# Kernel tuning notes

Measured on AMD Instinct MI355X. Metric: run time of the kernel, lower is better.

## Reference

```python
import jax, jax.numpy as jnp
import numpy as np

SEQ = 4096
R_DIM = 1024
Z_DIM = 1024
AT_DIM = 1024
G_DIM = 1024


def _xavier(key, shape):
    fan_in, fan_out = shape[1], shape[0]
    limit = float(np.sqrt(6.0 / (fan_in + fan_out)))
    return jax.random.uniform(key, shape, jnp.float32, -limit, limit)


def setup_inputs() -> dict:
    key = jax.random.key(0)
    ks = jax.random.split(key, 12)
    return {
        "R": jax.random.normal(ks[0], (SEQ, R_DIM), jnp.float32),
        "W_alpha": _xavier(ks[1], (R_DIM, 2 * R_DIM)),
        "b_alpha": jnp.zeros((R_DIM,), jnp.float32),
        "W_delta": _xavier(ks[2], (R_DIM, 2 * R_DIM)),
        "b_delta": jnp.zeros((R_DIM,), jnp.float32),
        "W_q": _xavier(ks[3], (AT_DIM, Z_DIM)),
        "b_q": jnp.zeros((AT_DIM,), jnp.float32),
        "W_k": _xavier(ks[4], (AT_DIM, Z_DIM)),
        "b_k": jnp.zeros((AT_DIM,), jnp.float32),
        "W_v": _xavier(ks[5], (AT_DIM, Z_DIM)),
        "b_v": jnp.zeros((AT_DIM,), jnp.float32),
        "W_z": _xavier(ks[6], (Z_DIM, R_DIM)),
        "b_z": jnp.zeros((Z_DIM,), jnp.float32),
        "W_f": _xavier(ks[7], (AT_DIM, G_DIM)),
        "b_f": jnp.zeros((AT_DIM,), jnp.float32),
        "W_EMA": _xavier(ks[8], (G_DIM, R_DIM)),
        "b_EMA": jnp.zeros((G_DIM,), jnp.float32),
        "W_z_at": _xavier(ks[9], (G_DIM, AT_DIM)),
        "b_z_at": jnp.zeros((G_DIM,), jnp.float32),
        "W_i": _xavier(ks[10], (1, R_DIM)),
        "b_i": jnp.zeros((1,), jnp.float32),
        "W_final": _xavier(ks[11], (1, G_DIM)),
    }


def reference(R, W_alpha, b_alpha, W_delta, b_delta, W_q, b_q, W_k, b_k,
              W_v, b_v, W_z, b_z, W_f, b_f, W_EMA, b_EMA, W_z_at, b_z_at,
              W_i, b_i, W_final):
    r_dim = R.shape[-1]
    at_dim = W_q.shape[0]
    # prepend zero row; r_t / r_{t-1} pairs
    R2 = jnp.concatenate([jnp.zeros((1, r_dim), R.dtype), R], axis=0)
    r_t, r_prev = R2[1:], R2[:-1]
    concat_r = jnp.concatenate([r_prev, r_t], axis=1)  # [m, 2r]
    alpha = jnp.tanh(concat_r @ W_alpha.T + b_alpha)
    delta = jnp.tanh(concat_r @ W_delta.T + b_delta)
    R_EMA = alpha * r_t + (1.0 - alpha) * delta * r_prev
    Z = jax.nn.silu(R_EMA @ W_z.T + b_z)
    Q = Z @ W_q.T + b_q
    K = Z @ W_k.T + b_k
    V = Z @ W_v.T + b_v
    scores = (Q @ K.T) / jnp.sqrt(jnp.float32(at_dim))  # [m, m]
    weights = jax.nn.softmax(scores, axis=-1)
    Z_at = weights @ V
    R_EMA_p = R_EMA @ W_EMA.T + b_EMA
    f = jax.nn.sigmoid(R_EMA_p @ W_f.T + b_f)
    Z_at_p = f * Z_at
    Z_EMA_f = Z_at_p @ W_z_at.T + b_z_at
    Z_tp = jnp.tanh(R_EMA_p + Z_EMA_f)
    i = jnp.tanh(R_EMA @ W_i.T + b_i)  # [m, 1]
    Z_final = i * Z_tp + (1.0 - i) * R_EMA_p
    p_hat = jax.nn.sigmoid(Z_final @ W_final.T)  # [m, 1]
    return p_hat
```

## Files before the change

kernel.cpp:

```cpp
#include <hip/hip_runtime.h>
#include <cstdint>
#include <cmath>

#define MB (1024ull * 1024ull)

typedef unsigned short u16;
typedef __attribute__((ext_vector_type(8))) short short8;
typedef __attribute__((ext_vector_type(4))) float f32x4;

enum { M_TANH = 0, M_ZRE = 1, M_QKV = 2, M_SIG = 3, M_SCALE = 4, M_PVMUL = 5, M_F32 = 6 };

__device__ __forceinline__ u16 f2b(float f) {
  union { float f; uint32_t u; } v; v.f = f;
  uint32_t r = v.u + 0x7FFFu + ((v.u >> 16) & 1u);
  return (u16)(r >> 16);
}
__device__ __forceinline__ float b2f(u16 u) {
  union { uint32_t u; float f; } v; v.u = ((uint32_t)u) << 16;
  return v.f;
}

typedef __attribute__((address_space(3))) uint32_t lds_u32;
typedef const __attribute__((address_space(1))) uint32_t glb_u32;

__device__ __forceinline__ void gload16(const void* g, void* l) {
  __builtin_amdgcn_global_load_lds((glb_u32*)g, (lds_u32*)l, 16, 0, 0);
}

template <int MODE, int BNT>
__global__ __launch_bounds__(256) void gemm(const u16* __restrict__ A,
                                            const u16* __restrict__ B,
                                            const float* __restrict__ bias,
                                            const u16* __restrict__ auxb,
                                            u16* __restrict__ Cb,
                                            u16* __restrict__ Cb2,
                                            float* __restrict__ Cf,
                                            int K, int lda, int ldb, float scale) {
  constexpr int NJ = (BNT == 128) ? 4 : 2;
  __shared__ u16 As[2][128 * 32];
  __shared__ u16 Bs[2][BNT * 32];
  const int tid = threadIdx.x;
  const int wid = tid >> 6, lane = tid & 63;

  const int gx = gridDim.x, nwg = gx * gridDim.y;
  int id = blockIdx.y * gx + blockIdx.x;
  if ((nwg & 7) == 0) id = (id & 7) * (nwg >> 3) + (id >> 3);
  const int bm = (id / gx) * 128, bn = (id % gx) * BNT;
  const int wm = wid >> 1, wn = wid & 1;

  const int srow = tid >> 2;
  const int schunk = (tid & 3) ^ ((srow >> 1) & 3);
  const u16* gA = A + (size_t)(bm + srow) * lda + schunk * 8;
  const u16* gB = B + (size_t)(bn + srow) * ldb + schunk * 8;

  f32x4 acc[4][NJ];
#pragma unroll
  for (int i = 0; i < 4; ++i)
#pragma unroll
    for (int j = 0; j < NJ; ++j) acc[i][j] = (f32x4){0.f, 0.f, 0.f, 0.f};

  const int ar = lane & 15;
  const int pch = (((lane >> 4) ^ ((ar >> 1) & 3))) * 8;

  const int NT = K >> 5;

  auto stage = [&](int buf, int t) {
    const u16* a = gA + (size_t)t * 32;
    const u16* b = gB + (size_t)t * 32;
    gload16(a, &As[buf][wid * 512]);
    gload16(a + (size_t)64 * lda, &As[buf][wid * 512 + 2048]);
    gload16(b, &Bs[buf][wid * 512]);
    if (BNT == 128) gload16(b + (size_t)64 * ldb, &Bs[buf][wid * 512 + 2048]);
  };

  stage(0, 0);
  __syncthreads();
  int cur = 0;
  for (int t = 0; t < NT; ++t) {
    if (t + 1 < NT) stage(cur ^ 1, t + 1);
    short8 af[4], bf[NJ];
#pragma unroll
    for (int i = 0; i < 4; ++i)
      af[i] = *reinterpret_cast<const short8*>(&As[cur][(wm * 64 + i * 16 + ar) * 32 + pch]);
#pragma unroll
    for (int j = 0; j < NJ; ++j)
      bf[j] = *reinterpret_cast<const short8*>(&Bs[cur][(wn * (BNT / 2) + j * 16 + ar) * 32 + pch]);
#pragma unroll
    for (int i = 0; i < 4; ++i)
#pragma unroll
      for (int j = 0; j < NJ; ++j)
        acc[i][j] = __builtin_amdgcn_mfma_f32_16x16x32_bf16(af[i], bf[j], acc[i][j], 0, 0, 0);
    __syncthreads();
    cur ^= 1;
  }

#pragma unroll
  for (int i = 0; i < 4; ++i) {
    const int rb = bm + wm * 64 + i * 16 + (lane >> 4) * 4;
#pragma unroll
    for (int j = 0; j < NJ; ++j) {
      const int n = bn + wn * (BNT / 2) + j * 16 + (lane & 15);
#pragma unroll
      for (int r = 0; r < 4; ++r) {
        const int m = rb + r;
        float v = acc[i][j][r];
        if (MODE == M_TANH) {
          v = tanhf(v + bias[n]);
          Cb[(size_t)m * 2048 + n] = f2b(v);
        } else if (MODE == M_ZRE) {
          v += bias[n];
          if (n < 1024) { const float s = v / (1.f + expf(-v)); Cb[(size_t)m * 1024 + n] = f2b(s); }
          else Cb2[(size_t)m * 1024 + (n - 1024)] = f2b(v);
        } else if (MODE == M_QKV) {
          v += bias[n];
          if (n < 2048) Cb[(size_t)m * 2048 + n] = f2b(v);
          else Cb2[(size_t)m * 1024 + (n - 2048)] = f2b(v);
        } else if (MODE == M_SIG) {
          v = 1.f / (1.f + expf(-(v + bias[n])));
          Cb[(size_t)m * 1024 + n] = f2b(v);
        } else if (MODE == M_SCALE) {
          Cb[(size_t)m * 4096 + n] = f2b(v * scale);
        } else if (MODE == M_PVMUL) {
          v *= b2f(auxb[(size_t)m * 1024 + n]);
          Cb[(size_t)m * 1024 + n] = f2b(v);
        } else if (MODE == M_F32) {
          Cf[(size_t)m * 1024 + n] = v + bias[n];
        }
      }
    }
  }
}

__global__ __launch_bounds__(256) void convert_all(
    const float* __restrict__ s0, const float* __restrict__ s1, const float* __restrict__ s2,
    const float* __restrict__ s3, const float* __restrict__ s4, const float* __restrict__ s5,
    const float* __restrict__ s6, const float* __restrict__ s7, const float* __restrict__ s8,
    u16* __restrict__ Wad, u16* __restrict__ Wze, u16* __restrict__ Wqkv,
    u16* __restrict__ Wfb, u16* __restrict__ Wzab) {
  const int idx = blockIdx.x * 256 + threadIdx.x;
  const float* src; u16* dst; int off;
  if      (idx < 524288)  { src = s0; dst = Wad;           off = idx; }
  else if (idx < 1048576) { src = s1; dst = Wad + 2097152; off = idx - 524288; }
  else if (idx < 1310720) { src = s2; dst = Wze;           off = idx - 1048576; }
  else if (idx < 1572864) { src = s3; dst = Wze + 1048576; off = idx - 1310720; }
  else if (idx < 1835008) { src = s4; dst = Wqkv;          off = idx - 1572864; }
  else if (idx < 2097152) { src = s5; dst = Wqkv + 1048576; off = idx - 1835008; }
  else if (idx < 2359296) { src = s6; dst = Wqkv + 2097152; off = idx - 2097152; }
  else if (idx < 2621440) { src = s7; dst = Wfb;           off = idx - 2359296; }
  else                    { src = s8; dst = Wzab;          off = idx - 2621440; }
  const float4 v = reinterpret_cast<const float4*>(src)[off];
  ushort4 o; o.x = f2b(v.x); o.y = f2b(v.y); o.z = f2b(v.z); o.w = f2b(v.w);
  reinterpret_cast<ushort4*>(dst)[off] = o;
}

__global__ void copy_bias(const float* __restrict__ ba, const float* __restrict__ bd,
                          const float* __restrict__ bz, const float* __restrict__ be,
                          const float* __restrict__ bq, const float* __restrict__ bk,
                          const float* __restrict__ bv,
                          float* __restrict__ bad, float* __restrict__ bze,
                          float* __restrict__ bqkv) {
  const int t = threadIdx.x;
  const float4* src; float4* dst;
  switch (blockIdx.x) {
    case 0: src = (const float4*)ba; dst = (float4*)bad; break;
    case 1: src = (const float4*)bd; dst = (float4*)(bad + 1024); break;
    case 2: src = (const float4*)bz; dst = (float4*)bze; break;
    case 3: src = (const float4*)be; dst = (float4*)(bze + 1024); break;
    case 4: src = (const float4*)bq; dst = (float4*)bqkv; break;
    case 5: src = (const float4*)bk; dst = (float4*)(bqkv + 1024); break;
    default: src = (const float4*)bv; dst = (float4*)(bqkv + 2048); break;
  }
  dst[t] = src[t];
}

__global__ __launch_bounds__(256) void concat_kern(const float* __restrict__ R,
                                                   u16* __restrict__ Rc) {
  const int idx = blockIdx.x * 256 + threadIdx.x;
  const int m = idx >> 9;
  const int c = (idx & 511) * 4;
  float4 v;
  if (c < 1024) {
    if (m > 0) v = *reinterpret_cast<const float4*>(&R[(size_t)(m - 1) * 1024 + c]);
    else v = make_float4(0.f, 0.f, 0.f, 0.f);
  } else {
    v = *reinterpret_cast<const float4*>(&R[(size_t)m * 1024 + (c - 1024)]);
  }
  ushort4 o; o.x = f2b(v.x); o.y = f2b(v.y); o.z = f2b(v.z); o.w = f2b(v.w);
  reinterpret_cast<ushort4*>(Rc)[idx] = o;
}

__global__ __launch_bounds__(256) void ema_combine(const float* __restrict__ R,
                                                   const u16* __restrict__ adb,
                                                   u16* __restrict__ REMA) {
  const int idx = blockIdx.x * 256 + threadIdx.x;
  const int m = idx >> 8, c4 = idx & 255;
  const float4 rt = reinterpret_cast<const float4*>(R)[idx];
  float4 rp = make_float4(0.f, 0.f, 0.f, 0.f);
  if (m > 0) rp = reinterpret_cast<const float4*>(R)[idx - 256];
  const ushort4 a4 = reinterpret_cast<const ushort4*>(adb)[m * 512 + c4];
  const ushort4 d4 = reinterpret_cast<const ushort4*>(adb)[m * 512 + 256 + c4];
  ushort4 o;
  { const float av = b2f(a4.x); o.x = f2b(av * rt.x + (1.f - av) * b2f(d4.x) * rp.x); }
  { const float av = b2f(a4.y); o.y = f2b(av * rt.y + (1.f - av) * b2f(d4.y) * rp.y); }
  { const float av = b2f(a4.z); o.z = f2b(av * rt.z + (1.f - av) * b2f(d4.z) * rp.z); }
  { const float av = b2f(a4.w); o.w = f2b(av * rt.w + (1.f - av) * b2f(d4.w) * rp.w); }
  reinterpret_cast<ushort4*>(REMA)[idx] = o;
}

__device__ __forceinline__ float waveMax(float v) {
#pragma unroll
  for (int o = 32; o; o >>= 1) v = fmaxf(v, __shfl_down(v, o));
  return v;
}
__device__ __forceinline__ float waveSum(float v) {
#pragma unroll
  for (int o = 32; o; o >>= 1) v += __shfl_down(v, o);
  return v;
}

__global__ __launch_bounds__(256) void softmax_rows(u16* __restrict__ S) {
  u16* p = S + (size_t)blockIdx.x * 4096;
  const int tid = threadIdx.x;
  float v[16];
#pragma unroll
  for (int j = 0; j < 4; ++j) {
    const ushort4 t = *reinterpret_cast<const ushort4*>(&p[tid * 4 + 1024 * j]);
    v[4 * j + 0] = b2f(t.x); v[4 * j + 1] = b2f(t.y);
    v[4 * j + 2] = b2f(t.z); v[4 * j + 3] = b2f(t.w);
  }
  float mx = -INFINITY;
#pragma unroll
  for (int j = 0; j < 16; ++j) mx = fmaxf(mx, v[j]);
  __shared__ float red[4];
  const float wm = waveMax(mx);
  if ((tid & 63) == 0) red[tid >> 6] = wm;
  __syncthreads();
  mx = fmaxf(fmaxf(red[0], red[1]), fmaxf(red[2], red[3]));
  __syncthreads();
  float sum = 0.f;
#pragma unroll
  for (int j = 0; j < 16; ++j) { v[j] = expf(v[j] - mx); sum += v[j]; }
  const float ws_ = waveSum(sum);
  if ((tid & 63) == 0) red[tid >> 6] = ws_;
  __syncthreads();
  const float inv = 1.f / (red[0] + red[1] + red[2] + red[3]);
#pragma unroll
  for (int j = 0; j < 4; ++j) {
    ushort4 t;
    t.x = f2b(v[4 * j + 0] * inv); t.y = f2b(v[4 * j + 1] * inv);
    t.z = f2b(v[4 * j + 2] * inv); t.w = f2b(v[4 * j + 3] * inv);
    *reinterpret_cast<ushort4*>(&p[tid * 4 + 1024 * j]) = t;
  }
}

__global__ __launch_bounds__(256) void transpose_b16(const u16* __restrict__ V,
                                                     u16* __restrict__ Vt) {
  __shared__ u16 t[64][72];
  const int bn = blockIdx.x * 64;
  const int bk = blockIdx.y * 64;
  const int tx = threadIdx.x & 15, ty = threadIdx.x >> 4;
#pragma unroll
  for (int i = 0; i < 64; i += 16) {
    const ushort4 v = *reinterpret_cast<const ushort4*>(&V[(size_t)(bk + ty + i) * 1024 + bn + tx * 4]);
    t[ty + i][tx * 4 + 0] = v.x; t[ty + i][tx * 4 + 1] = v.y;
    t[ty + i][tx * 4 + 2] = v.z; t[ty + i][tx * 4 + 3] = v.w;
  }
  __syncthreads();
#pragma unroll
  for (int i = 0; i < 64; i += 16) {
    ushort4 w;
    w.x = t[tx * 4 + 0][ty + i]; w.y = t[tx * 4 + 1][ty + i];
    w.z = t[tx * 4 + 2][ty + i]; w.w = t[tx * 4 + 3][ty + i];
    *reinterpret_cast<ushort4*>(&Vt[(size_t)(bn + ty + i) * 4096 + bk + tx * 4]) = w;
  }
}

__global__ void final_kern(const u16* __restrict__ REMAb, const u16* __restrict__ REMApb,
                           const float* __restrict__ ZEMAf,
                           const float* __restrict__ Wi, const float* __restrict__ bi,
                           const float* __restrict__ Wfin, float* __restrict__ out) {
  const int m = blockIdx.x, l = threadIdx.x;
  float si = 0.f;
#pragma unroll
  for (int j = 0; j < 16; ++j) {
    const int n = l + 64 * j;
    si += b2f(REMAb[(size_t)m * 1024 + n]) * Wi[n];
  }
#pragma unroll
  for (int o = 32; o; o >>= 1) si += __shfl_xor(si, o);
  const float im = tanhf(si + bi[0]);
  float s = 0.f;
#pragma unroll
  for (int j = 0; j < 16; ++j) {
    const int n = l + 64 * j;
    const float rp = b2f(REMApb[(size_t)m * 1024 + n]);
    const float zf = im * tanhf(rp + ZEMAf[(size_t)m * 1024 + n]) + (1.f - im) * rp;
    s += zf * Wfin[n];
  }
#pragma unroll
  for (int o = 32; o; o >>= 1) s += __shfl_down(s, o);
  if (l == 0) out[m] = 1.f / (1.f + expf(-s));
}

extern "C" void kernel_launch(void* const* d_in, const int* in_sizes, int n_in,
                              void* d_out, int out_size, void* d_ws, size_t ws_size,
                              hipStream_t stream) {
  const float* R       = (const float*)d_in[0];
  const float* W_alpha = (const float*)d_in[1];  const float* b_alpha = (const float*)d_in[2];
  const float* W_delta = (const float*)d_in[3];  const float* b_delta = (const float*)d_in[4];
  const float* W_q     = (const float*)d_in[5];  const float* b_q     = (const float*)d_in[6];
  const float* W_k     = (const float*)d_in[7];  const float* b_k     = (const float*)d_in[8];
  const float* W_v     = (const float*)d_in[9];  const float* b_v     = (const float*)d_in[10];
  const float* W_z     = (const float*)d_in[11]; const float* b_z     = (const float*)d_in[12];
  const float* W_f     = (const float*)d_in[13]; const float* b_f     = (const float*)d_in[14];
  const float* W_EMA   = (const float*)d_in[15]; const float* b_EMA   = (const float*)d_in[16];
  const float* W_z_at  = (const float*)d_in[17]; const float* b_z_at  = (const float*)d_in[18];
  const float* W_i     = (const float*)d_in[19]; const float* b_i     = (const float*)d_in[20];
  const float* W_final = (const float*)d_in[21];
  float* out = (float*)d_out;
  uint8_t* w8 = (uint8_t*)d_ws;

  u16*   Rc     = (u16*)(w8 + 0 * MB);
  u16*   Zb     = (u16*)(w8 + 0 * MB);
  u16*   REMApb = (u16*)(w8 + 8 * MB);
  u16*   Wad    = (u16*)(w8 + 16 * MB);
  u16*   fvb    = (u16*)(w8 + 16 * MB);
  u16*   adb    = (u16*)(w8 + 24 * MB);
  float* ZEMAf  = (float*)(w8 + 24 * MB);
  u16*   Wqkv   = (u16*)(w8 + 40 * MB);
  u16*   Vtb    = (u16*)(w8 + 40 * MB);
  u16*   Wze    = (u16*)(w8 + 46 * MB);
  u16*   Wfb    = (u16*)(w8 + 50 * MB);
  u16*   Wzab   = (u16*)(w8 + 52 * MB);
  u16*   REMAb  = (u16*)(w8 + 54 * MB);
  u16*   QKb    = (u16*)(w8 + 62 * MB);
  u16*   Zatpb  = (u16*)(w8 + 62 * MB);
  u16*   Vb     = (u16*)(w8 + 78 * MB);
  u16*   Sb     = (u16*)(w8 + 78 * MB);
  float* bad    = (float*)(w8 + 110 * MB + 64 * 1024);
  float* bze    = bad + 2048;
  float* bqkv   = bze + 2048;

  const dim3 blk(256);
  convert_all<<<11264, blk, 0, stream>>>(W_alpha, W_delta, W_z, W_EMA, W_q, W_k, W_v, W_f, W_z_at,
                                         Wad, Wze, Wqkv, Wfb, Wzab);
  concat_kern<<<8192, blk, 0, stream>>>(R, Rc);
  copy_bias<<<7, blk, 0, stream>>>(b_alpha, b_delta, b_z, b_EMA, b_q, b_k, b_v, bad, bze, bqkv);

  gemm<M_TANH, 128><<<dim3(16, 32), blk, 0, stream>>>(Rc, Wad, bad, nullptr, adb, nullptr, nullptr, 2048, 2048, 2048, 1.f);
  ema_combine<<<4096, blk, 0, stream>>>(R, adb, REMAb);
  gemm<M_ZRE, 128><<<dim3(16, 32), blk, 0, stream>>>(REMAb, Wze, bze, nullptr, Zb, REMApb, nullptr, 1024, 1024, 1024, 1.f);
  gemm<M_QKV, 128><<<dim3(24, 32), blk, 0, stream>>>(Zb, Wqkv, bqkv, nullptr, QKb, Vb, nullptr, 1024, 1024, 1024, 1.f);
  gemm<M_SIG, 64><<<dim3(16, 32), blk, 0, stream>>>(REMApb, Wfb, b_f, nullptr, fvb, nullptr, nullptr, 1024, 1024, 1024, 1.f);
  transpose_b16<<<dim3(16, 64), blk, 0, stream>>>(Vb, Vtb);
  gemm<M_SCALE, 128><<<dim3(32, 32), blk, 0, stream>>>(QKb, QKb + 1024, nullptr, nullptr, Sb, nullptr, nullptr, 1024, 2048, 2048, 0.03125f);
  softmax_rows<<<4096, blk, 0, stream>>>(Sb);
  gemm<M_PVMUL, 64><<<dim3(16, 32), blk, 0, stream>>>(Sb, Vtb, nullptr, fvb, Zatpb, nullptr, nullptr, 4096, 4096, 4096, 1.f);
  gemm<M_F32, 64><<<dim3(16, 32), blk, 0, stream>>>(Zatpb, Wzab, b_z_at, nullptr, nullptr, nullptr, ZEMAf, 1024, 1024, 1024, 1.f);
  final_kern<<<4096, 64, 0, stream>>>(REMAb, REMApb, ZEMAf, W_i, b_i, W_final, out);
}
```

Baseline: 345.6 us.

## Use 64-row GEMM tiles, merge gate GEMM into QKV, split-K the PV product

The GEMM template gains a configurable M tile. Several GEMMs now use 64x128 tiles, which doubles the workgroup count so more CUs are busy. The sigmoid gate GEMM is folded into the QKV launch as extra column blocks that read different A/B/bias pointers, saving one launch. The long-K PV GEMM is split into two K halves that write fp32 partials, followed by a reduce kernel that sums them and applies the gate. In exchange it adds fp32 partial traffic and an extra kernel, and smaller tiles mean less operand reuse per block.

Measured after the change: 340.7 us. Within noise of the previous version (-1.4%).

```diff
diff --git a/kernel.cpp b/kernel.cpp
--- a/kernel.cpp
+++ b/kernel.cpp
@@ -8,7 +8,7 @@
 typedef __attribute__((ext_vector_type(8))) short short8;
 typedef __attribute__((ext_vector_type(4))) float f32x4;
 
-enum { M_TANH = 0, M_ZRE = 1, M_QKV = 2, M_SIG = 3, M_SCALE = 4, M_PVMUL = 5, M_F32 = 6 };
+enum { M_TANH = 0, M_ZRE = 1, M_QKVF = 2, M_SCALE = 3, M_PVRAW = 4, M_F32 = 5 };
 
 __device__ __forceinline__ u16 f2b(float f) {
   union { float f; uint32_t u; } v; v.f = f;
@@ -27,17 +27,25 @@
   __builtin_amdgcn_global_load_lds((glb_u32*)g, (lds_u32*)l, 16, 0, 0);
 }
 
-template <int MODE, int BNT>
+template <int MODE, int BMT, int BNT>
 __global__ __launch_bounds__(256) void gemm(const u16* __restrict__ A,
                                             const u16* __restrict__ B,
                                             const float* __restrict__ bias,
-                                            const u16* __restrict__ auxb,
+                                            const u16* __restrict__ A2,
+                                            const u16* __restrict__ B2,
+                                            const float* __restrict__ bias2,
                                             u16* __restrict__ Cb,
                                             u16* __restrict__ Cb2,
+                                            u16* __restrict__ Cb3,
                                             float* __restrict__ Cf,
                                             int K, int lda, int ldb, float scale) {
-  constexpr int NJ = (BNT == 128) ? 4 : 2;
-  __shared__ u16 As[2][128 * 32];
+  constexpr int WN = (BMT == 64 && BNT == 128) ? 4 : 2;
+  constexpr int WM = 4 / WN;
+  constexpr int WR = BMT / WM;
+  constexpr int WC = BNT / WN;
+  constexpr int NI = WR / 16;
+  constexpr int NJ = WC / 16;
+  __shared__ u16 As[2][BMT * 32];
   __shared__ u16 Bs[2][BNT * 32];
   const int tid = threadIdx.x;
   const int wid = tid >> 6, lane = tid & 63;
@@ -45,17 +53,24 @@
   const int gx = gridDim.x, nwg = gx * gridDim.y;
   int id = blockIdx.y * gx + blockIdx.x;
   if ((nwg & 7) == 0) id = (id & 7) * (nwg >> 3) + (id >> 3);
-  const int bm = (id / gx) * 128, bn = (id % gx) * BNT;
-  const int wm = wid >> 1, wn = wid & 1;
+  const int bm = (id / gx) * BMT, bn = (id % gx) * BNT;
+  const int wm = wid / WN, wn = wid % WN;
+  const int rowbase = wm * WR, colbase = wn * WC;
+
+  const bool isf = (MODE == M_QKVF) && (bn >= 3072);
+  const u16* Ab = isf ? A2 : A;
+  const u16* Bb = isf ? B2 : B;
+  const int bnl = isf ? bn - 3072 : bn;
+  const int kofs = (MODE == M_PVRAW) ? (int)blockIdx.z * K : 0;
 
   const int srow = tid >> 2;
   const int schunk = (tid & 3) ^ ((srow >> 1) & 3);
-  const u16* gA = A + (size_t)(bm + srow) * lda + schunk * 8;
-  const u16* gB = B + (size_t)(bn + srow) * ldb + schunk * 8;
-
-  f32x4 acc[4][NJ];
-#pragma unroll
-  for (int i = 0; i < 4; ++i)
+  const u16* gA = Ab + (size_t)(bm + srow) * lda + kofs + schunk * 8;
+  const u16* gB = Bb + (size_t)(bnl + srow) * ldb + kofs + schunk * 8;
+
+  f32x4 acc[NI][NJ];
+#pragma unroll
+  for (int i = 0; i < NI; ++i)
 #pragma unroll
     for (int j = 0; j < NJ; ++j) acc[i][j] = (f32x4){0.f, 0.f, 0.f, 0.f};
 
@@ -68,7 +83,7 @@
     const u16* a = gA + (size_t)t * 32;
     const u16* b = gB + (size_t)t * 32;
     gload16(a, &As[buf][wid * 512]);
-    gload16(a + (size_t)64 * lda, &As[buf][wid * 512 + 2048]);
+    if (BMT == 128) gload16(a + (size_t)64 * lda, &As[buf][wid * 512 + 2048]);
     gload16(b, &Bs[buf][wid * 512]);
     if (BNT == 128) gload16(b + (size_t)64 * ldb, &Bs[buf][wid * 512 + 2048]);
   };
@@ -78,15 +93,15 @@
   int cur = 0;
   for (int t = 0; t < NT; ++t) {
     if (t + 1 < NT) stage(cur ^ 1, t + 1);
-    short8 af[4], bf[NJ];
-#pragma unroll
-    for (int i = 0; i < 4; ++i)
-      af[i] = *reinterpret_cast<const short8*>(&As[cur][(wm * 64 + i * 16 + ar) * 32 + pch]);
+    short8 af[NI], bf[NJ];
+#pragma unroll
+    for (int i = 0; i < NI; ++i)
+      af[i] = *reinterpret_cast<const short8*>(&As[cur][(rowbase + i * 16 + ar) * 32 + pch]);
 #pragma unroll
     for (int j = 0; j < NJ; ++j)
-      bf[j] = *reinterpret_cast<const short8*>(&Bs[cur][(wn * (BNT / 2) + j * 16 + ar) * 32 + pch]);
-#pragma unroll
-    for (int i = 0; i < 4; ++i)
+      bf[j] = *reinterpret_cast<const short8*>(&Bs[cur][(colbase + j * 16 + ar) * 32 + pch]);
+#pragma unroll
+    for (int i = 0; i < NI; ++i)
 #pragma unroll
       for (int j = 0; j < NJ; ++j)
         acc[i][j] = __builtin_amdgcn_mfma_f32_16x16x32_bf16(af[i], bf[j], acc[i][j], 0, 0, 0);
@@ -94,12 +109,15 @@
     cur ^= 1;
   }
 
-#pragma unroll
-  for (int i = 0; i < 4; ++i) {
-    const int rb = bm + wm * 64 + i * 16 + (lane >> 4) * 4;
+  float* Cfz = Cf;
+  if (MODE == M_PVRAW && blockIdx.z != 0) Cfz = (float*)Cb3;
+
+#pragma unroll
+  for (int i = 0; i < NI; ++i) {
+    const int rb = bm + rowbase + i * 16 + (lane >> 4) * 4;
 #pragma unroll
     for (int j = 0; j < NJ; ++j) {
-      const int n = bn + wn * (BNT / 2) + j * 16 + (lane & 15);
+      const int n = bn + colbase + j * 16 + (lane & 15);
 #pragma unroll
       for (int r = 0; r < 4; ++r) {
         const int m = rb + r;
@@ -111,24 +129,42 @@
           v += bias[n];
           if (n < 1024) { const float s = v / (1.f + expf(-v)); Cb[(size_t)m * 1024 + n] = f2b(s); }
           else Cb2[(size_t)m * 1024 + (n - 1024)] = f2b(v);
-        } else if (MODE == M_QKV) {
-          v += bias[n];
-          if (n < 2048) Cb[(size_t)m * 2048 + n] = f2b(v);
-          else Cb2[(size_t)m * 1024 + (n - 2048)] = f2b(v);
-        } else if (MODE == M_SIG) {
-          v = 1.f / (1.f + expf(-(v + bias[n])));
-          Cb[(size_t)m * 1024 + n] = f2b(v);
+        } else if (MODE == M_QKVF) {
+          if (isf) {
+            const int nl = n - 3072;
+            const float s = 1.f / (1.f + expf(-(v + bias2[nl])));
+            Cb3[(size_t)m * 1024 + nl] = f2b(s);
+          } else {
+            v += bias[n];
+            if (n < 2048) Cb[(size_t)m * 2048 + n] = f2b(v);
+            else Cb2[(size_t)m * 1024 + (n - 2048)] = f2b(v);
+          }
         } else if (MODE == M_SCALE) {
           Cb[(size_t)m * 4096 + n] = f2b(v * scale);
-        } else if (MODE == M_PVMUL) {
-          v *= b2f(auxb[(size_t)m * 1024 + n]);
-          Cb[(size_t)m * 1024 + n] = f2b(v);
+        } else if (MODE == M_PVRAW) {
+          Cfz[(size_t)m * 1024 + n] = v;
         } else if (MODE == M_F32) {
           Cf[(size_t)m * 1024 + n] = v + bias[n];
         }
       }
     }
   }
+}
+
+__global__ __launch_bounds__(256) void pv_reduce(const float* __restrict__ p0,
+                                                 const float* __restrict__ p1,
+                                                 const u16* __restrict__ fvb,
+                                                 u16* __restrict__ Zatp) {
+  const int idx = blockIdx.x * 256 + threadIdx.x;
+  const float4 a = reinterpret_cast<const float4*>(p0)[idx];
+  const float4 b = reinterpret_cast<const float4*>(p1)[idx];
+  const ushort4 f4 = reinterpret_cast<const ushort4*>(fvb)[idx];
+  ushort4 o;
+  o.x = f2b((a.x + b.x) * b2f(f4.x));
+  o.y = f2b((a.y + b.y) * b2f(f4.y));
+  o.z = f2b((a.z + b.z) * b2f(f4.z));
+  o.w = f2b((a.w + b.w) * b2f(f4.w));
+  reinterpret_cast<ushort4*>(Zatp)[idx] = o;
 }
 
 __global__ __launch_bounds__(256) void convert_all(
@@ -322,10 +358,12 @@
 
   u16*   Rc     = (u16*)(w8 + 0 * MB);
   u16*   Zb     = (u16*)(w8 + 0 * MB);
+  u16*   Zatpb  = (u16*)(w8 + 0 * MB);
   u16*   REMApb = (u16*)(w8 + 8 * MB);
   u16*   Wad    = (u16*)(w8 + 16 * MB);
   u16*   fvb    = (u16*)(w8 + 16 * MB);
   u16*   adb    = (u16*)(w8 + 24 * MB);
+  float* pvp0   = (float*)(w8 + 24 * MB);
   float* ZEMAf  = (float*)(w8 + 24 * MB);
   u16*   Wqkv   = (u16*)(w8 + 40 * MB);
   u16*   Vtb    = (u16*)(w8 + 40 * MB);
@@ -334,7 +372,7 @@
   u16*   Wzab   = (u16*)(w8 + 52 * MB);
   u16*   REMAb  = (u16*)(w8 + 54 * MB);
   u16*   QKb    = (u16*)(w8 + 62 * MB);
-  u16*   Zatpb  = (u16*)(w8 + 62 * MB);
+  float* pvp1   = (float*)(w8 + 62 * MB);
   u16*   Vb     = (u16*)(w8 + 78 * MB);
   u16*   Sb     = (u16*)(w8 + 78 * MB);
   float* bad    = (float*)(w8 + 110 * MB + 64 * 1024);
@@ -347,15 +385,21 @@
   concat_kern<<<8192, blk, 0, stream>>>(R, Rc);
   copy_bias<<<7, blk, 0, stream>>>(b_alpha, b_delta, b_z, b_EMA, b_q, b_k, b_v, bad, bze, bqkv);
 
-  gemm<M_TANH, 128><<<dim3(16, 32), blk, 0, stream>>>(Rc, Wad, bad, nullptr, adb, nullptr, nullptr, 2048, 2048, 2048, 1.f);
+  gemm<M_TANH, 64, 128><<<dim3(16, 64), blk, 0, stream>>>(
+      Rc, Wad, bad, nullptr, nullptr, nullptr, adb, nullptr, nullptr, nullptr, 2048, 2048, 2048, 1.f);
   ema_combine<<<4096, blk, 0, stream>>>(R, adb, REMAb);
-  gemm<M_ZRE, 128><<<dim3(16, 32), blk, 0, stream>>>(REMAb, Wze, bze, nullptr, Zb, REMApb, nullptr, 1024, 1024, 1024, 1.f);
-  gemm<M_QKV, 128><<<dim3(24, 32), blk, 0, stream>>>(Zb, Wqkv, bqkv, nullptr, QKb, Vb, nullptr, 1024, 1024, 1024, 1.f);
-  gemm<M_SIG, 64><<<dim3(16, 32), blk, 0, stream>>>(REMApb, Wfb, b_f, nullptr, fvb, nullptr, nullptr, 1024, 1024, 1024, 1.f);
+  gemm<M_ZRE, 64, 128><<<dim3(16, 64), blk, 0, stream>>>(
+      REMAb, Wze, bze, nullptr, nullptr, nullptr, Zb, REMApb, nullptr, nullptr, 1024, 1024, 1024, 1.f);
+  gemm<M_QKVF, 64, 128><<<dim3(32, 64), blk, 0, stream>>>(
+      Zb, Wqkv, bqkv, REMApb, Wfb, b_f, QKb, Vb, fvb, nullptr, 1024, 1024, 1024, 1.f);
   transpose_b16<<<dim3(16, 64), blk, 0, stream>>>(Vb, Vtb);
-  gemm<M_SCALE, 128><<<dim3(32, 32), blk, 0, stream>>>(QKb, QKb + 1024, nullptr, nullptr, Sb, nullptr, nullptr, 1024, 2048, 2048, 0.03125f);
+  gemm<M_SCALE, 128, 128><<<dim3(32, 32), blk, 0, stream>>>(
+      QKb, QKb + 1024, nullptr, nullptr, nullptr, nullptr, Sb, nullptr, nullptr, nullptr, 1024, 2048, 2048, 0.03125f);
   softmax_rows<<<4096, blk, 0, stream>>>(Sb);
-  gemm<M_PVMUL, 64><<<dim3(16, 32), blk, 0, stream>>>(Sb, Vtb, nullptr, fvb, Zatpb, nullptr, nullptr, 4096, 4096, 4096, 1.f);
-  gemm<M_F32, 64><<<dim3(16, 32), blk, 0, stream>>>(Zatpb, Wzab, b_z_at, nullptr, nullptr, nullptr, ZEMAf, 1024, 1024, 1024, 1.f);
+  gemm<M_PVRAW, 128, 64><<<dim3(16, 32, 2), blk, 0, stream>>>(
+      Sb, Vtb, nullptr, nullptr, nullptr, nullptr, nullptr, nullptr, (u16*)pvp1, pvp0, 2048, 4096, 4096, 1.f);
+  pv_reduce<<<4096, blk, 0, stream>>>(pvp0, pvp1, fvb, Zatpb);
+  gemm<M_F32, 64, 128><<<dim3(8, 64), blk, 0, stream>>>(
+      Zatpb, Wzab, b_z_at, nullptr, nullptr, nullptr, nullptr, nullptr, nullptr, ZEMAf, 1024, 1024, 1024, 1.f);
   final_kern<<<4096, 64, 0, stream>>>(REMAb, REMApb, ZEMAf, W_i, b_i, W_final, out);
 }
```
